# Performance work log

Measured on AMD Instinct MI355X. Metric: run time of the kernel, lower is better.

The kernel has to match this reference:

```python
import jax, jax.numpy as jnp
import numpy as np

HIDDEN = 1024
TILE = 128


def setup_inputs() -> dict:
    key = jax.random.key(0)
    ks = jax.random.split(key, 9)
    B, S, D = 2, 4096, HIDDEN
    s = 1.0 / np.sqrt(D)
    return {
        "batch": jax.random.normal(ks[0], (B, S, D), jnp.float32),
        "Wq": jax.random.normal(ks[1], (D, D), jnp.float32) * s,
        "bq": jax.random.normal(ks[2], (D,), jnp.float32) * 0.01,
        "Wk": jax.random.normal(ks[3], (D, D), jnp.float32) * s,
        "bk": jax.random.normal(ks[4], (D,), jnp.float32) * 0.01,
        "Wv": jax.random.normal(ks[5], (D, D), jnp.float32) * s,
        "bv": jax.random.normal(ks[6], (D,), jnp.float32) * 0.01,
        "Wo": jax.random.normal(ks[7], (D, D), jnp.float32) * s,
        "bo": jax.random.normal(ks[8], (D,), jnp.float32) * 0.01,
    }


def reference(batch, Wq, bq, Wk, bk, Wv, bv, Wo, bo):
    B, S, D = batch.shape
    scale = 1.0 / np.sqrt(D)
    T = S // TILE  # seq_len chosen divisible by tile size

    # Projections (nn.Linear: x @ W.T + b)
    q = batch @ Wq.T + bq
    k = batch @ Wk.T + bk
    v = batch @ Wv.T + bv

    # Tile K/V along the sequence axis: [B, T, TILE, D]
    k_t = k.reshape(B, T, TILE, D)
    v_t = v.reshape(B, T, TILE, D)

    # Per-tile scores and per-tile softmax (NOT a global softmax —
    # faithful to the module, which normalizes within each kv tile).
    scores = jnp.einsum("bqd,btkd->btqk", q, k_t) * scale  # [B, T, S, TILE]
    w = jax.nn.softmax(scores, axis=-1)

    # Sum of per-tile attention outputs over kv tiles
    out = jnp.einsum("btqk,btkd->bqd", w, v_t)  # [B, S, D]

    # Normalizing factor: sum of per-tile softmax weights (== T analytically,
    # computed explicitly to match the original math bit-for-bit in spirit)
    norm = w.sum(axis=-1).sum(axis=1)[..., None]  # [B, S, 1]
    out = out / (norm + 1e-6)

    return out @ Wo.T + bo
```

## Files before the change

### kernel.cpp

```cpp
#include <hip/hip_runtime.h>


#define D_ 1024
#define S_ 4096
#define B_ 2

typedef unsigned short u16;
typedef float f32x4 __attribute__((ext_vector_type(4)));
typedef float float4v __attribute__((ext_vector_type(4)));
typedef __bf16 bf16x8 __attribute__((ext_vector_type(8)));
typedef unsigned short us8 __attribute__((ext_vector_type(8)));

static __device__ __forceinline__ u16 f2bf(float f) {
    unsigned int u = __builtin_bit_cast(unsigned int, f);
    u += 0x7FFFu + ((u >> 16) & 1u);
    return (u16)(u >> 16);
}

static __device__ __forceinline__ void gld16(const u16* g, u16* l) {
    __builtin_amdgcn_global_load_lds(
        (const __attribute__((address_space(1))) void*)g,
        (__attribute__((address_space(3))) void*)l, 16, 0, 0);
}

template <int N>
static __device__ __forceinline__ void waitv() {
    if constexpr (N == 0)      asm volatile("s_waitcnt vmcnt(0)" ::: "memory");
    else if constexpr (N == 2) asm volatile("s_waitcnt vmcnt(2)" ::: "memory");
    else if constexpr (N == 6) asm volatile("s_waitcnt vmcnt(6)" ::: "memory");
}

static __device__ __forceinline__ void lgkm0sb() {
    asm volatile("s_waitcnt lgkmcnt(0)" ::: "memory");
    __builtin_amdgcn_sched_barrier(0);
}

static __device__ __forceinline__ void xcd_map(int& bx, int& by) {
    const int gx = gridDim.x, gy = gridDim.y;
    int lin = blockIdx.x + blockIdx.y * gx;
    int ry = gy >> 3;
    int idx = lin >> 3;
    int q = idx / ry;
    bx = q;
    by = (lin & 7) * ry + (idx - q * ry);
}

__global__ void cast_kernel(const float* __restrict__ in, u16* __restrict__ out, int n8) {
    int i = blockIdx.x * blockDim.x + threadIdx.x;
    int stride = gridDim.x * blockDim.x;
    for (; i < n8; i += stride) {
        const float4v* p = (const float4v*)in + 2 * (size_t)i;
        float4v a = p[0], b = p[1];
        us8 o;
        o[0] = f2bf(a[0]); o[1] = f2bf(a[1]); o[2] = f2bf(a[2]); o[3] = f2bf(a[3]);
        o[4] = f2bf(b[0]); o[5] = f2bf(b[1]); o[6] = f2bf(b[2]); o[7] = f2bf(b[3]);
        *((us8*)out + i) = o;
    }
}

__global__ void cast4_kernel(const float* __restrict__ w0, const float* __restrict__ w1,
                             const float* __restrict__ w2, const float* __restrict__ w3,
                             u16* __restrict__ out, int n8per) {
    const float* srcs[4] = {w0, w1, w2, w3};
    const float* in = srcs[blockIdx.y];
    u16* o = out + (size_t)blockIdx.y * (size_t)n8per * 8;
    int i = blockIdx.x * blockDim.x + threadIdx.x;
    int stride = gridDim.x * blockDim.x;
    for (; i < n8per; i += stride) {
        const float4v* p = (const float4v*)in + 2 * (size_t)i;
        float4v a = p[0], b = p[1];
        us8 v;
        v[0] = f2bf(a[0]); v[1] = f2bf(a[1]); v[2] = f2bf(a[2]); v[3] = f2bf(a[3]);
        v[4] = f2bf(b[0]); v[5] = f2bf(b[1]); v[6] = f2bf(b[2]); v[7] = f2bf(b[3]);
        *((us8*)o + i) = v;
    }
}

__global__ void concat_bias(const float* __restrict__ b0, const float* __restrict__ b1,
                            const float* __restrict__ b2, float* __restrict__ out) {
    int i = blockIdx.x * 256 + threadIdx.x;
    const float* s = (i < 1024) ? b0 : ((i < 2048) ? b1 : b2);
    out[i] = s[i & 1023];
}

__global__ void transpose_v(const u16* __restrict__ V, u16* __restrict__ Vt, int ldv) {
    __shared__ u16 t[64][72];
    const int tid = threadIdx.x;
    const int d0 = blockIdx.x * 64;
    const int s0 = blockIdx.y * 64;
    const u16* Vb = V + (size_t)blockIdx.z * ((size_t)S_ * ldv);
    u16* Vtb = Vt + (size_t)blockIdx.z * ((size_t)D_ * S_);
#pragma unroll
    for (int it = 0; it < 2; it++) {
        int idx = it * 256 + tid;
        int row = idx >> 3;
        int ch = idx & 7;
        us8 v = *(const us8*)&Vb[(size_t)(s0 + row) * ldv + d0 + ch * 8];
        *(us8*)&t[row][ch * 8] = v;
    }
    __syncthreads();
#pragma unroll
    for (int it = 0; it < 2; it++) {
        int idx = it * 256 + tid;
        int jj = idx >> 3;
        int ch = idx & 7;
        us8 v;
#pragma unroll
        for (int e = 0; e < 8; e++) v[e] = t[ch * 8 + e][jj];
        *(us8*)&Vtb[(size_t)(d0 + jj) * S_ + s0 + ch * 8] = v;
    }
}

#define MMQ(ACC, MB, NB)                                                      \
    {                                                                         \
        _Pragma("unroll") for (int mi_ = 0; mi_ < 4; ++mi_) {                 \
            _Pragma("unroll") for (int ni_ = 0; ni_ < 2; ++ni_) {             \
                _Pragma("unroll") for (int kh_ = 0; kh_ < 2; ++kh_) {         \
                    ACC[(MB) + mi_][(NB) + ni_] =                             \
                        __builtin_amdgcn_mfma_f32_16x16x32_bf16(              \
                            af[mi_][kh_], bf[ni_][kh_],                       \
                            ACC[(MB) + mi_][(NB) + ni_], 0, 0, 0);            \
                }                                                             \
            }                                                                 \
        }                                                                     \
    }

__global__ __launch_bounds__(512, 1) void gemm_sm256(
    const u16* __restrict__ A, const u16* __restrict__ B, u16* __restrict__ C,
    int K, int lda, int ldb, int ldc, long sA, long sB, long sC)
{
    __shared__ u16 lA[2][256 * 64];
    __shared__ u16 lB[2][256 * 64];
    __shared__ float sred[2][8][128];
    const int tid = threadIdx.x, lane = tid & 63, wid = tid >> 6;
    const int wr = wid >> 2, wc = wid & 3;
    const int ar = lane & 15, sl = lane >> 4;
    const int z = blockIdx.z;
    A += (size_t)z * sA;
    B += (size_t)z * sB;
    int bx, by;
    xcd_map(bx, by);
    const int m0 = by * 256, n0 = bx * 256;
    const int NT = K >> 6, NI = NT >> 1;

    f32x4 acc[8][4];
#pragma unroll
    for (int i = 0; i < 8; i++)
#pragma unroll
        for (int j = 0; j < 4; j++)
#pragma unroll
            for (int r = 0; r < 4; r++) acc[i][j][r] = 0.0f;

    auto stg = [&](const u16* __restrict__ M, int ld, int mb, u16* ld0, int t, int h) {
#pragma unroll
        for (int j = 0; j < 2; ++j) {
            const int u = j * 512 + wid * 64 + lane;
            const int row = h * 128 + (u >> 3);
            const int ls = (u & 7) ^ (row & 7);
            gld16(M + (size_t)(mb + row) * ld + (t << 6) + ls * 8, ld0 + h * 8192 + u * 8);
        }
    };
    auto rd = [&](const u16* l, int R, int kh) -> bf16x8 {
        const int ps = ((kh << 2) | sl) ^ (R & 7);
        return *(const bf16x8*)&l[R * 64 + ps * 8];
    };

    stg(A, lda, m0, lA[0], 0, 0); stg(A, lda, m0, lA[0], 0, 1);
    stg(B, ldb, n0, lB[0], 0, 0); stg(B, ldb, n0, lB[0], 0, 1);
    stg(A, lda, m0, lA[1], 1, 0);
    waitv<2>();
    __builtin_amdgcn_s_barrier();

    bf16x8 af[4][2], bf[2][2];
    for (int j = 0; j < NI; ++j) {
        const int a = 2 * j, b = a + 1;
        const bool s2 = (j + 1 < NI);
#pragma unroll
        for (int mi = 0; mi < 4; ++mi)
#pragma unroll
            for (int kh = 0; kh < 2; ++kh)
                af[mi][kh] = rd(lA[0], wr * 128 + mi * 16 + ar, kh);
#pragma unroll
        for (int ni = 0; ni < 2; ++ni)
#pragma unroll
            for (int kh = 0; kh < 2; ++kh)
                bf[ni][kh] = rd(lB[0], wc * 64 + ni * 16 + ar, kh);
        stg(A, lda, m0, lA[1], b, 1);
        lgkm0sb();
        __builtin_amdgcn_s_setprio(1);
        MMQ(acc, 0, 0);
        __builtin_amdgcn_s_setprio(0);
        __builtin_amdgcn_s_barrier();
#pragma unroll
        for (int ni = 0; ni < 2; ++ni)
#pragma unroll
            for (int kh = 0; kh < 2; ++kh)
                bf[ni][kh] = rd(lB[0], wc * 64 + (2 + ni) * 16 + ar, kh);
        stg(B, ldb, n0, lB[1], b, 0);
        lgkm0sb();
        __builtin_amdgcn_s_setprio(1);
        MMQ(acc, 0, 2);
        __builtin_amdgcn_s_setprio(0);
        __builtin_amdgcn_s_barrier();
#pragma unroll
        for (int mi = 0; mi < 4; ++mi)
#pragma unroll
            for (int kh = 0; kh < 2; ++kh)
                af[mi][kh] = rd(lA[0], wr * 128 + (4 + mi) * 16 + ar, kh);
        stg(B, ldb, n0, lB[1], b, 1);
        lgkm0sb();
        __builtin_amdgcn_s_setprio(1);
        MMQ(acc, 4, 2);
        __builtin_amdgcn_s_setprio(0);
        __builtin_amdgcn_s_barrier();
#pragma unroll
        for (int ni = 0; ni < 2; ++ni)
#pragma unroll
            for (int kh = 0; kh < 2; ++kh)
                bf[ni][kh] = rd(lB[0], wc * 64 + ni * 16 + ar, kh);
        if (s2) stg(A, lda, m0, lA[0], a + 2, 0);
        lgkm0sb();
        __builtin_amdgcn_s_setprio(1);
        MMQ(acc, 4, 0);
        __builtin_amdgcn_s_setprio(0);
        if (s2) waitv<2>(); else waitv<0>();
        __builtin_amdgcn_s_barrier();
#pragma unroll
        for (int mi = 0; mi < 4; ++mi)
#pragma unroll
            for (int kh = 0; kh < 2; ++kh)
                af[mi][kh] = rd(lA[1], wr * 128 + mi * 16 + ar, kh);
#pragma unroll
        for (int ni = 0; ni < 2; ++ni)
#pragma unroll
            for (int kh = 0; kh < 2; ++kh)
                bf[ni][kh] = rd(lB[1], wc * 64 + ni * 16 + ar, kh);
        if (s2) stg(B, ldb, n0, lB[0], a + 2, 0);
        lgkm0sb();
        __builtin_amdgcn_s_setprio(1);
        MMQ(acc, 0, 0);
        __builtin_amdgcn_s_setprio(0);
        __builtin_amdgcn_s_barrier();
#pragma unroll
        for (int ni = 0; ni < 2; ++ni)
#pragma unroll
            for (int kh = 0; kh < 2; ++kh)
                bf[ni][kh] = rd(lB[1], wc * 64 + (2 + ni) * 16 + ar, kh);
        if (s2) stg(B, ldb, n0, lB[0], a + 2, 1);
        lgkm0sb();
        __builtin_amdgcn_s_setprio(1);
        MMQ(acc, 0, 2);
        __builtin_amdgcn_s_setprio(0);
        __builtin_amdgcn_s_barrier();
#pragma unroll
        for (int mi = 0; mi < 4; ++mi)
#pragma unroll
            for (int kh = 0; kh < 2; ++kh)
                af[mi][kh] = rd(lA[1], wr * 128 + (4 + mi) * 16 + ar, kh);
        if (s2) stg(A, lda, m0, lA[0], a + 2, 1);
        lgkm0sb();
        __builtin_amdgcn_s_setprio(1);
        MMQ(acc, 4, 2);
        __builtin_amdgcn_s_setprio(0);
        __builtin_amdgcn_s_barrier();
#pragma unroll
        for (int ni = 0; ni < 2; ++ni)
#pragma unroll
            for (int kh = 0; kh < 2; ++kh)
                bf[ni][kh] = rd(lB[1], wc * 64 + ni * 16 + ar, kh);
        if (s2) stg(A, lda, m0, lA[1], b + 2, 0);
        lgkm0sb();
        __builtin_amdgcn_s_setprio(1);
        MMQ(acc, 4, 0);
        __builtin_amdgcn_s_setprio(0);
        if (s2) waitv<2>(); else waitv<0>();
        __builtin_amdgcn_s_barrier();
    }

    const float SL = 0.03125f * 1.44269504088896341f;
#pragma unroll
    for (int mi = 0; mi < 8; mi++) {
#pragma unroll
        for (int r = 0; r < 4; r++) {
            float m = acc[mi][0][r];
#pragma unroll
            for (int ni = 1; ni < 4; ni++) m = fmaxf(m, acc[mi][ni][r]);
            m = fmaxf(m, __shfl_xor(m, 1));
            m = fmaxf(m, __shfl_xor(m, 2));
            m = fmaxf(m, __shfl_xor(m, 4));
            m = fmaxf(m, __shfl_xor(m, 8));
            if (ar == 0) sred[0][wid][mi * 16 + sl * 4 + r] = m;
        }
    }
    __syncthreads();
#pragma unroll
    for (int mi = 0; mi < 8; mi++) {
#pragma unroll
        for (int r = 0; r < 4; r++) {
            const int rl = mi * 16 + sl * 4 + r;
            const float mc = fmaxf(sred[0][wid][rl], sred[0][wid ^ 1][rl]);
            float s = 0.0f;
#pragma unroll
            for (int ni = 0; ni < 4; ni++) {
                float e = exp2f((acc[mi][ni][r] - mc) * SL);
                acc[mi][ni][r] = e;
                s += e;
            }
            s += __shfl_xor(s, 1);
            s += __shfl_xor(s, 2);
            s += __shfl_xor(s, 4);
            s += __shfl_xor(s, 8);
            if (ar == 0) sred[1][wid][rl] = s;
        }
    }
    __syncthreads();
    u16* Cp = C + (size_t)z * sC;
#pragma unroll
    for (int mi = 0; mi < 8; mi++) {
#pragma unroll
        for (int r = 0; r < 4; r++) {
            const int rl = mi * 16 + sl * 4 + r;
            const float inv = 1.0f / (sred[1][wid][rl] + sred[1][wid ^ 1][rl]);
            const int row = m0 + wr * 128 + rl;
#pragma unroll
            for (int ni = 0; ni < 4; ni++)
                Cp[(size_t)row * ldc + n0 + wc * 64 + ni * 16 + ar] =
                    f2bf(acc[mi][ni][r] * inv);
        }
    }
}

template <int EPI>
__global__ __launch_bounds__(512, 1) void gemm128(
    const u16* __restrict__ A, const u16* __restrict__ B, void* __restrict__ Cv,
    const float* __restrict__ bias, int K, int lda, int ldb, int ldc,
    long sA, long sB, long sC, float scale)
{
    __shared__ u16 lA[3][128 * 64];
    __shared__ u16 lB[3][256 * 64];
    const int tid = threadIdx.x, lane = tid & 63, wid = tid >> 6;
    const int wr = wid >> 2, wc = wid & 3;
    const int ar = lane & 15, sl = lane >> 4;
    const int z = blockIdx.z;
    A += (size_t)z * sA;
    B += (size_t)z * sB;
    int bx, by;
    xcd_map(bx, by);
    const int m0 = by * 128, n0 = bx * 256;
    const int NT = K >> 6;

    f32x4 acc[4][4];
#pragma unroll
    for (int i = 0; i < 4; i++)
#pragma unroll
        for (int j = 0; j < 4; j++)
#pragma unroll
            for (int r = 0; r < 4; r++) acc[i][j][r] = 0.0f;

    auto stgA = [&](int t) {
        u16* dst = &lA[t % 3][0];
#pragma unroll
        for (int j = 0; j < 2; ++j) {
            const int u = j * 512 + wid * 64 + lane;
            const int row = u >> 3;
            const int ls = (u & 7) ^ (row & 7);
            gld16(A + (size_t)(m0 + row) * lda + (t << 6) + ls * 8, dst + u * 8);
        }
    };
    auto stgB = [&](int t, int h) {
        u16* dst = &lB[t % 3][0];
#pragma unroll
        for (int j = 0; j < 2; ++j) {
            const int u = j * 512 + wid * 64 + lane;
            const int row = h * 128 + (u >> 3);
            const int ls = (u & 7) ^ (row & 7);
            gld16(B + (size_t)(n0 + row) * ldb + (t << 6) + ls * 8, dst + h * 8192 + u * 8);
        }
    };
    auto rd = [&](const u16* l, int R, int kh) -> bf16x8 {
        const int ps = ((kh << 2) | sl) ^ (R & 7);
        return *(const bf16x8*)&l[R * 64 + ps * 8];
    };

    stgA(0); stgB(0, 0); stgB(0, 1);
    stgA(1); stgB(1, 0); stgB(1, 1);
    waitv<6>();
    __builtin_amdgcn_s_barrier();

    bf16x8 af[4][2], bf[2][2];
    for (int t = 0; t < NT; ++t) {
        const u16* bufA = &lA[t % 3][0];
        const u16* bufB = &lB[t % 3][0];
        const bool s2 = (t + 2 < NT);
#pragma unroll
        for (int mi = 0; mi < 4; ++mi)
#pragma unroll
            for (int kh = 0; kh < 2; ++kh)
                af[mi][kh] = rd(bufA, wr * 64 + mi * 16 + ar, kh);
#pragma unroll
        for (int ni = 0; ni < 2; ++ni)
#pragma unroll
            for (int kh = 0; kh < 2; ++kh)
                bf[ni][kh] = rd(bufB, wc * 64 + ni * 16 + ar, kh);
        if (s2) { stgA(t + 2); stgB(t + 2, 0); }
        lgkm0sb();
        __builtin_amdgcn_s_setprio(1);
        MMQ(acc, 0, 0);
        __builtin_amdgcn_s_setprio(0);
        __builtin_amdgcn_s_barrier();
#pragma unroll
        for (int ni = 0; ni < 2; ++ni)
#pragma unroll
            for (int kh = 0; kh < 2; ++kh)
                bf[ni][kh] = rd(bufB, wc * 64 + (2 + ni) * 16 + ar, kh);
        if (s2) stgB(t + 2, 1);
        lgkm0sb();
        __builtin_amdgcn_s_setprio(1);
        MMQ(acc, 0, 2);
        __builtin_amdgcn_s_setprio(0);
        if (s2) waitv<6>(); else waitv<0>();
        __builtin_amdgcn_s_barrier();
    }

#pragma unroll
    for (int mi = 0; mi < 4; mi++) {
#pragma unroll
        for (int ni = 0; ni < 4; ni++) {
            const int col = n0 + wc * 64 + ni * 16 + ar;
            const int rowb = m0 + wr * 64 + mi * 16 + sl * 4;
            if constexpr (EPI == 0) {
                u16* C = (u16*)Cv + (size_t)z * sC;
                const float bv = bias[col];
#pragma unroll
                for (int r = 0; r < 4; r++)
                    C[(size_t)(rowb + r) * ldc + col] = f2bf(acc[mi][ni][r] + bv);
            } else if constexpr (EPI == 1) {
                u16* C = (u16*)Cv + (size_t)z * sC;
#pragma unroll
                for (int r = 0; r < 4; r++)
                    C[(size_t)(rowb + r) * ldc + col] = f2bf(acc[mi][ni][r] * scale);
            } else {
                float* C = (float*)Cv + (size_t)z * sC;
                const float bv = bias[col];
#pragma unroll
                for (int r = 0; r < 4; r++)
                    C[(size_t)(rowb + r) * ldc + col] = acc[mi][ni][r] + bv;
            }
        }
    }
}

extern "C" void kernel_launch(void* const* d_in, const int* in_sizes, int n_in,
                              void* d_out, int out_size, void* d_ws, size_t ws_size,
                              hipStream_t stream)
{
    const float* X  = (const float*)d_in[0];
    const float* Wq = (const float*)d_in[1];
    const float* bq = (const float*)d_in[2];
    const float* Wk = (const float*)d_in[3];
    const float* bk = (const float*)d_in[4];
    const float* Wv = (const float*)d_in[5];
    const float* bv = (const float*)d_in[6];
    const float* Wo = (const float*)d_in[7];
    const float* bo = (const float*)d_in[8];
    float* OUT = (float*)d_out;

    u16* ws = (u16*)d_ws;
    const size_t NTOK = (size_t)B_ * S_;
    const size_t XSZ = NTOK * D_;
    u16* Xb   = ws;
    u16* QKVb = Xb + XSZ;
    u16* Vt   = QKVb + NTOK * (size_t)(3 * D_);
    u16* Wqb  = Vt + XSZ;
    u16* Wsm  = Wqb + (size_t)4 * D_ * D_;
    float* bqkv = (float*)(Wsm + (size_t)B_ * S_ * S_);
    u16* Ob   = Xb;

    u16* Qp = QKVb;
    u16* Kp = QKVb + D_;
    u16* Vp = QKVb + 2 * D_;
    const int ldqkv = 3 * D_;

    cast_kernel<<<dim3(2048), dim3(256), 0, stream>>>(X, Xb, (int)(XSZ / 8));
    cast4_kernel<<<dim3(512, 4), dim3(256), 0, stream>>>(Wq, Wk, Wv, Wo, Wqb,
                                                         (int)((size_t)D_ * D_ / 8));
    concat_bias<<<dim3(12), dim3(256), 0, stream>>>(bq, bk, bv, bqkv);

    gemm128<0><<<dim3(3 * D_ / 256, NTOK / 128, 1), 512, 0, stream>>>(
        Xb, Wqb, QKVb, bqkv, D_, D_, D_, ldqkv, 0, 0, 0, 1.0f);

    transpose_v<<<dim3(D_ / 64, S_ / 64, B_), 256, 0, stream>>>(Vp, Vt, ldqkv);

    gemm_sm256<<<dim3(S_ / 256, S_ / 256, B_), 512, 0, stream>>>(
        Qp, Kp, Wsm, D_, ldqkv, ldqkv, S_,
        (long)S_ * ldqkv, (long)S_ * ldqkv, (long)S_ * S_);

    gemm128<1><<<dim3(D_ / 256, S_ / 128, B_), 512, 0, stream>>>(
        Wsm, Vt, Ob, nullptr, S_, S_, S_, D_,
        (long)S_ * S_, (long)D_ * S_, (long)S_ * D_, 1.0f / (32.0f + 1e-6f));

    gemm128<2><<<dim3(D_ / 256, NTOK / 128, 1), 512, 0, stream>>>(
        Ob, Wqb + (size_t)3 * D_ * D_, OUT, bo, D_, D_, D_, D_, 0, 0, 0, 1.0f);
}
```

Before: 372.7 us.

## Generalize 256x256 GEMM with full B-fragment reuse and use it for QKV projection

The 256x256 softmax GEMM becomes a templated gemm256 with an epilogue switch. Its inner loop now loads all four B fragments once per K-step and reuses them across both A halves instead of reloading B, with precomputed staging and read addresses and a reordered prefetch schedule. The QKV projection moves from the 128-row GEMM to this 256x256 tile kernel, halving its grid. This cuts LDS traffic and raises per-block reuse, at the cost of more registers held for fragments and fewer blocks for the projection.

```diff
diff --git a/kernel.cpp b/kernel.cpp
--- a/kernel.cpp
+++ b/kernel.cpp
@@ -26,7 +26,6 @@
 template <int N>
 static __device__ __forceinline__ void waitv() {
     if constexpr (N == 0)      asm volatile("s_waitcnt vmcnt(0)" ::: "memory");
-    else if constexpr (N == 2) asm volatile("s_waitcnt vmcnt(2)" ::: "memory");
     else if constexpr (N == 6) asm volatile("s_waitcnt vmcnt(6)" ::: "memory");
 }
 
@@ -111,23 +110,25 @@
     }
 }
 
-#define MMQ(ACC, MB, NB)                                                      \
+#define MM8(MI0, NI0)                                                         \
     {                                                                         \
         _Pragma("unroll") for (int mi_ = 0; mi_ < 4; ++mi_) {                 \
             _Pragma("unroll") for (int ni_ = 0; ni_ < 2; ++ni_) {             \
                 _Pragma("unroll") for (int kh_ = 0; kh_ < 2; ++kh_) {         \
-                    ACC[(MB) + mi_][(NB) + ni_] =                             \
+                    acc[(MI0) + mi_][(NI0) + ni_] =                           \
                         __builtin_amdgcn_mfma_f32_16x16x32_bf16(              \
-                            af[mi_][kh_], bf[ni_][kh_],                       \
-                            ACC[(MB) + mi_][(NB) + ni_], 0, 0, 0);            \
+                            af[(MI0) + mi_][kh_], bf[(NI0) + ni_][kh_],       \
+                            acc[(MI0) + mi_][(NI0) + ni_], 0, 0, 0);          \
                 }                                                             \
             }                                                                 \
         }                                                                     \
     }
 
-__global__ __launch_bounds__(512, 1) void gemm_sm256(
-    const u16* __restrict__ A, const u16* __restrict__ B, u16* __restrict__ C,
-    int K, int lda, int ldb, int ldc, long sA, long sB, long sC)
+template <int EPI>
+__global__ __launch_bounds__(512, 1) void gemm256(
+    const u16* __restrict__ A, const u16* __restrict__ B, void* __restrict__ Cv,
+    const float* __restrict__ bias, int K, int lda, int ldb, int ldc,
+    long sA, long sB, long sC)
 {
     __shared__ u16 lA[2][256 * 64];
     __shared__ u16 lB[2][256 * 64];
@@ -151,181 +152,180 @@
 #pragma unroll
             for (int r = 0; r < 4; r++) acc[i][j][r] = 0.0f;
 
-    auto stg = [&](const u16* __restrict__ M, int ld, int mb, u16* ld0, int t, int h) {
-#pragma unroll
-        for (int j = 0; j < 2; ++j) {
-            const int u = j * 512 + wid * 64 + lane;
-            const int row = h * 128 + (u >> 3);
-            const int ls = (u & 7) ^ (row & 7);
-            gld16(M + (size_t)(mb + row) * ld + (t << 6) + ls * 8, ld0 + h * 8192 + u * 8);
-        }
-    };
-    auto rd = [&](const u16* l, int R, int kh) -> bf16x8 {
-        const int ps = ((kh << 2) | sl) ^ (R & 7);
-        return *(const bf16x8*)&l[R * 64 + ps * 8];
-    };
-
-    stg(A, lda, m0, lA[0], 0, 0); stg(A, lda, m0, lA[0], 0, 1);
-    stg(B, ldb, n0, lB[0], 0, 0); stg(B, ldb, n0, lB[0], 0, 1);
-    stg(A, lda, m0, lA[1], 1, 0);
-    waitv<2>();
+    const int uS = wid * 64 + lane;
+    const int rS = uS >> 3;
+    const int lsS = (lane & 7) ^ (rS & 7);
+    const u16* pA = A + (size_t)(m0 + rS) * lda + lsS * 8;
+    const u16* pB = B + (size_t)(n0 + rS) * ldb + lsS * 8;
+    auto stgA = [&](int t, int h) {
+        u16* dst = &lA[t & 1][h * 8192 + uS * 8];
+        const u16* src = pA + (size_t)h * 128 * lda + (t << 6);
+        gld16(src, dst);
+        gld16(src + (size_t)64 * lda, dst + 4096);
+    };
+    auto stgB = [&](int t, int h) {
+        u16* dst = &lB[t & 1][h * 8192 + uS * 8];
+        const u16* src = pB + (size_t)h * 128 * ldb + (t << 6);
+        gld16(src, dst);
+        gld16(src + (size_t)64 * ldb, dst + 4096);
+    };
+    const int psk0 = (sl ^ (ar & 7)) * 8;
+    const int psk1 = ((4 | sl) ^ (ar & 7)) * 8;
+    const int aoff = wr * 8192 + ar * 64;
+    const int boff = (wc >> 1) * 8192 + (wc & 1) * 4096 + ar * 64;
+    auto rdA = [&](int buf, int mi, int kh) -> bf16x8 {
+        return *(const bf16x8*)&lA[buf][aoff + mi * 1024 + (kh ? psk1 : psk0)];
+    };
+    auto rdB = [&](int buf, int ni, int kh) -> bf16x8 {
+        return *(const bf16x8*)&lB[buf][boff + ni * 1024 + (kh ? psk1 : psk0)];
+    };
+
+    stgA(0, 0); stgA(0, 1); stgB(0, 0); stgB(0, 1);
+    stgB(1, 0); stgB(1, 1); stgA(1, 0);
+    waitv<6>();
     __builtin_amdgcn_s_barrier();
 
-    bf16x8 af[4][2], bf[2][2];
+    bf16x8 af[8][2], bf[4][2];
     for (int j = 0; j < NI; ++j) {
         const int a = 2 * j, b = a + 1;
-        const bool s2 = (j + 1 < NI);
+        const bool more = (j + 1 < NI);
 #pragma unroll
         for (int mi = 0; mi < 4; ++mi)
 #pragma unroll
-            for (int kh = 0; kh < 2; ++kh)
-                af[mi][kh] = rd(lA[0], wr * 128 + mi * 16 + ar, kh);
-#pragma unroll
-        for (int ni = 0; ni < 2; ++ni)
-#pragma unroll
-            for (int kh = 0; kh < 2; ++kh)
-                bf[ni][kh] = rd(lB[0], wc * 64 + ni * 16 + ar, kh);
-        stg(A, lda, m0, lA[1], b, 1);
+            for (int kh = 0; kh < 2; ++kh) af[mi][kh] = rdA(0, mi, kh);
+#pragma unroll
+        for (int ni = 0; ni < 4; ++ni)
+#pragma unroll
+            for (int kh = 0; kh < 2; ++kh) bf[ni][kh] = rdB(0, ni, kh);
+        stgA(b, 1);
         lgkm0sb();
         __builtin_amdgcn_s_setprio(1);
-        MMQ(acc, 0, 0);
-        __builtin_amdgcn_s_setprio(0);
-        __builtin_amdgcn_s_barrier();
-#pragma unroll
-        for (int ni = 0; ni < 2; ++ni)
-#pragma unroll
-            for (int kh = 0; kh < 2; ++kh)
-                bf[ni][kh] = rd(lB[0], wc * 64 + (2 + ni) * 16 + ar, kh);
-        stg(B, ldb, n0, lB[1], b, 0);
+        MM8(0, 0);
+        __builtin_amdgcn_s_setprio(0);
+        __builtin_amdgcn_s_barrier();
+#pragma unroll
+        for (int mi = 4; mi < 8; ++mi)
+#pragma unroll
+            for (int kh = 0; kh < 2; ++kh) af[mi][kh] = rdA(0, mi, kh);
+        if (more) stgB(a + 2, 0);
         lgkm0sb();
         __builtin_amdgcn_s_setprio(1);
-        MMQ(acc, 0, 2);
-        __builtin_amdgcn_s_setprio(0);
+        MM8(4, 0);
+        __builtin_amdgcn_s_setprio(0);
+        __builtin_amdgcn_s_barrier();
+        if (more) stgB(a + 2, 1);
+        __builtin_amdgcn_s_setprio(1);
+        MM8(0, 2);
+        __builtin_amdgcn_s_setprio(0);
+        __builtin_amdgcn_s_barrier();
+        if (more) stgA(a + 2, 0);
+        __builtin_amdgcn_s_setprio(1);
+        MM8(4, 2);
+        __builtin_amdgcn_s_setprio(0);
+        if (more) waitv<6>(); else waitv<0>();
         __builtin_amdgcn_s_barrier();
 #pragma unroll
         for (int mi = 0; mi < 4; ++mi)
 #pragma unroll
-            for (int kh = 0; kh < 2; ++kh)
-                af[mi][kh] = rd(lA[0], wr * 128 + (4 + mi) * 16 + ar, kh);
-        stg(B, ldb, n0, lB[1], b, 1);
+            for (int kh = 0; kh < 2; ++kh) af[mi][kh] = rdA(1, mi, kh);
+#pragma unroll
+        for (int ni = 0; ni < 4; ++ni)
+#pragma unroll
+            for (int kh = 0; kh < 2; ++kh) bf[ni][kh] = rdB(1, ni, kh);
+        if (more) stgA(a + 2, 1);
         lgkm0sb();
         __builtin_amdgcn_s_setprio(1);
-        MMQ(acc, 4, 2);
-        __builtin_amdgcn_s_setprio(0);
-        __builtin_amdgcn_s_barrier();
-#pragma unroll
-        for (int ni = 0; ni < 2; ++ni)
-#pragma unroll
-            for (int kh = 0; kh < 2; ++kh)
-                bf[ni][kh] = rd(lB[0], wc * 64 + ni * 16 + ar, kh);
-        if (s2) stg(A, lda, m0, lA[0], a + 2, 0);
+        MM8(0, 0);
+        __builtin_amdgcn_s_setprio(0);
+        __builtin_amdgcn_s_barrier();
+#pragma unroll
+        for (int mi = 4; mi < 8; ++mi)
+#pragma unroll
+            for (int kh = 0; kh < 2; ++kh) af[mi][kh] = rdA(1, mi, kh);
+        if (more) stgB(b + 2, 0);
         lgkm0sb();
         __builtin_amdgcn_s_setprio(1);
-        MMQ(acc, 4, 0);
-        __builtin_amdgcn_s_setprio(0);
-        if (s2) waitv<2>(); else waitv<0>();
-        __builtin_amdgcn_s_barrier();
-#pragma unroll
-        for (int mi = 0; mi < 4; ++mi)
-#pragma unroll
-            for (int kh = 0; kh < 2; ++kh)
-                af[mi][kh] = rd(lA[1], wr * 128 + mi * 16 + ar, kh);
-#pragma unroll
-        for (int ni = 0; ni < 2; ++ni)
-#pragma unroll
-            for (int kh = 0; kh < 2; ++kh)
-                bf[ni][kh] = rd(lB[1], wc * 64 + ni * 16 + ar, kh);
-        if (s2) stg(B, ldb, n0, lB[0], a + 2, 0);
-        lgkm0sb();
-        __builtin_amdgcn_s_setprio(1);
-        MMQ(acc, 0, 0);
-        __builtin_amdgcn_s_setprio(0);
-        __builtin_amdgcn_s_barrier();
-#pragma unroll
-        for (int ni = 0; ni < 2; ++ni)
-#pragma unroll
-            for (int kh = 0; kh < 2; ++kh)
-                bf[ni][kh] = rd(lB[1], wc * 64 + (2 + ni) * 16 + ar, kh);
-        if (s2) stg(B, ldb, n0, lB[0], a + 2, 1);
-        lgkm0sb();
-        __builtin_amdgcn_s_setprio(1);
-        MMQ(acc, 0, 2);
-        __builtin_amdgcn_s_setprio(0);
-        __builtin_amdgcn_s_barrier();
-#pragma unroll
-        for (int mi = 0; mi < 4; ++mi)
-#pragma unroll
-            for (int kh = 0; kh < 2; ++kh)
-                af[mi][kh] = rd(lA[1], wr * 128 + (4 + mi) * 16 + ar, kh);
-        if (s2) stg(A, lda, m0, lA[0], a + 2, 1);
-        lgkm0sb();
-        __builtin_amdgcn_s_setprio(1);
-        MMQ(acc, 4, 2);
-        __builtin_amdgcn_s_setprio(0);
-        __builtin_amdgcn_s_barrier();
-#pragma unroll
-        for (int ni = 0; ni < 2; ++ni)
-#pragma unroll
-            for (int kh = 0; kh < 2; ++kh)
-                bf[ni][kh] = rd(lB[1], wc * 64 + ni * 16 + ar, kh);
-        if (s2) stg(A, lda, m0, lA[1], b + 2, 0);
-        lgkm0sb();
-        __builtin_amdgcn_s_setprio(1);
-        MMQ(acc, 4, 0);
-        __builtin_amdgcn_s_setprio(0);
-        if (s2) waitv<2>(); else waitv<0>();
-        __builtin_amdgcn_s_barrier();
-    }
-
-    const float SL = 0.03125f * 1.44269504088896341f;
-#pragma unroll
-    for (int mi = 0; mi < 8; mi++) {
-#pragma unroll
-        for (int r = 0; r < 4; r++) {
-            float m = acc[mi][0][r];
-#pragma unroll
-            for (int ni = 1; ni < 4; ni++) m = fmaxf(m, acc[mi][ni][r]);
-            m = fmaxf(m, __shfl_xor(m, 1));
-            m = fmaxf(m, __shfl_xor(m, 2));
-            m = fmaxf(m, __shfl_xor(m, 4));
-            m = fmaxf(m, __shfl_xor(m, 8));
-            if (ar == 0) sred[0][wid][mi * 16 + sl * 4 + r] = m;
-        }
-    }
-    __syncthreads();
-#pragma unroll
-    for (int mi = 0; mi < 8; mi++) {
-#pragma unroll
-        for (int r = 0; r < 4; r++) {
-            const int rl = mi * 16 + sl * 4 + r;
-            const float mc = fmaxf(sred[0][wid][rl], sred[0][wid ^ 1][rl]);
-            float s = 0.0f;
+        MM8(4, 0);
+        __builtin_amdgcn_s_setprio(0);
+        __builtin_amdgcn_s_barrier();
+        if (more) stgB(b + 2, 1);
+        __builtin_amdgcn_s_setprio(1);
+        MM8(0, 2);
+        __builtin_amdgcn_s_setprio(0);
+        __builtin_amdgcn_s_barrier();
+        if (more) stgA(b + 2, 0);
+        __builtin_amdgcn_s_setprio(1);
+        MM8(4, 2);
+        __builtin_amdgcn_s_setprio(0);
+        if (more) waitv<6>(); else waitv<0>();
+        __builtin_amdgcn_s_barrier();
+    }
+
+    if constexpr (EPI == 3) {
+        const float SL = 0.03125f * 1.44269504088896341f;
+#pragma unroll
+        for (int mi = 0; mi < 8; mi++) {
+#pragma unroll
+            for (int r = 0; r < 4; r++) {
+                float m = acc[mi][0][r];
+#pragma unroll
+                for (int ni = 1; ni < 4; ni++) m = fmaxf(m, acc[mi][ni][r]);
+                m = fmaxf(m, __shfl_xor(m, 1));
+                m = fmaxf(m, __shfl_xor(m, 2));
+                m = fmaxf(m, __shfl_xor(m, 4));
+                m = fmaxf(m, __shfl_xor(m, 8));
+                if (ar == 0) sred[0][wid][mi * 16 + sl * 4 + r] = m;
+            }
+        }
+        __syncthreads();
+#pragma unroll
+        for (int mi = 0; mi < 8; mi++) {
+#pragma unroll
+            for (int r = 0; r < 4; r++) {
+                const int rl = mi * 16 + sl * 4 + r;
+                const float mc = fmaxf(sred[0][wid][rl], sred[0][wid ^ 1][rl]);
+                float s = 0.0f;
+#pragma unroll
+                for (int ni = 0; ni < 4; ni++) {
+                    float e = exp2f((acc[mi][ni][r] - mc) * SL);
+                    acc[mi][ni][r] = e;
+                    s += e;
+                }
+                s += __shfl_xor(s, 1);
+                s += __shfl_xor(s, 2);
+                s += __shfl_xor(s, 4);
+                s += __shfl_xor(s, 8);
+                if (ar == 0) sred[1][wid][rl] = s;
+            }
+        }
+        __syncthreads();
+        u16* C = (u16*)Cv + (size_t)z * sC;
+#pragma unroll
+        for (int mi = 0; mi < 8; mi++) {
+#pragma unroll
+            for (int r = 0; r < 4; r++) {
+                const int rl = mi * 16 + sl * 4 + r;
+                const float inv = 1.0f / (sred[1][wid][rl] + sred[1][wid ^ 1][rl]);
+                const int row = m0 + wr * 128 + rl;
+#pragma unroll
+                for (int ni = 0; ni < 4; ni++)
+                    C[(size_t)row * ldc + n0 + wc * 64 + ni * 16 + ar] =
+                        f2bf(acc[mi][ni][r] * inv);
+            }
+        }
+    } else {
+        u16* C = (u16*)Cv + (size_t)z * sC;
+#pragma unroll
+        for (int mi = 0; mi < 8; mi++) {
 #pragma unroll
             for (int ni = 0; ni < 4; ni++) {
-                float e = exp2f((acc[mi][ni][r] - mc) * SL);
-                acc[mi][ni][r] = e;
-                s += e;
+                const int col = n0 + wc * 64 + ni * 16 + ar;
+                const int rowb = m0 + wr * 128 + mi * 16 + sl * 4;
+                const float bv = bias[col];
+#pragma unroll
+                for (int r = 0; r < 4; r++)
+                    C[(size_t)(rowb + r) * ldc + col] = f2bf(acc[mi][ni][r] + bv);
             }
-            s += __shfl_xor(s, 1);
-            s += __shfl_xor(s, 2);
-            s += __shfl_xor(s, 4);
-            s += __shfl_xor(s, 8);
-            if (ar == 0) sred[1][wid][rl] = s;
-        }
-    }
-    __syncthreads();
-    u16* Cp = C + (size_t)z * sC;
-#pragma unroll
-    for (int mi = 0; mi < 8; mi++) {
-#pragma unroll
-        for (int r = 0; r < 4; r++) {
-            const int rl = mi * 16 + sl * 4 + r;
-            const float inv = 1.0f / (sred[1][wid][rl] + sred[1][wid ^ 1][rl]);
-            const int row = m0 + wr * 128 + rl;
-#pragma unroll
-            for (int ni = 0; ni < 4; ni++)
-                Cp[(size_t)row * ldc + n0 + wc * 64 + ni * 16 + ar] =
-                    f2bf(acc[mi][ni][r] * inv);
         }
     }
 }
@@ -405,7 +405,14 @@
         if (s2) { stgA(t + 2); stgB(t + 2, 0); }
         lgkm0sb();
         __builtin_amdgcn_s_setprio(1);
-        MMQ(acc, 0, 0);
+#pragma unroll
+        for (int mi = 0; mi < 4; ++mi)
+#pragma unroll
+            for (int ni = 0; ni < 2; ++ni)
+#pragma unroll
+                for (int kh = 0; kh < 2; ++kh)
+                    acc[mi][ni] = __builtin_amdgcn_mfma_f32_16x16x32_bf16(
+                        af[mi][kh], bf[ni][kh], acc[mi][ni], 0, 0, 0);
         __builtin_amdgcn_s_setprio(0);
         __builtin_amdgcn_s_barrier();
 #pragma unroll
@@ -416,7 +423,14 @@
         if (s2) stgB(t + 2, 1);
         lgkm0sb();
         __builtin_amdgcn_s_setprio(1);
-        MMQ(acc, 0, 2);
+#pragma unroll
+        for (int mi = 0; mi < 4; ++mi)
+#pragma unroll
+            for (int ni = 0; ni < 2; ++ni)
+#pragma unroll
+                for (int kh = 0; kh < 2; ++kh)
+                    acc[mi][2 + ni] = __builtin_amdgcn_mfma_f32_16x16x32_bf16(
+                        af[mi][kh], bf[ni][kh], acc[mi][2 + ni], 0, 0, 0);
         __builtin_amdgcn_s_setprio(0);
         if (s2) waitv<6>(); else waitv<0>();
         __builtin_amdgcn_s_barrier();
@@ -428,13 +442,7 @@
         for (int ni = 0; ni < 4; ni++) {
             const int col = n0 + wc * 64 + ni * 16 + ar;
             const int rowb = m0 + wr * 64 + mi * 16 + sl * 4;
-            if constexpr (EPI == 0) {
-                u16* C = (u16*)Cv + (size_t)z * sC;
-                const float bv = bias[col];
-#pragma unroll
-                for (int r = 0; r < 4; r++)
-                    C[(size_t)(rowb + r) * ldc + col] = f2bf(acc[mi][ni][r] + bv);
-            } else if constexpr (EPI == 1) {
+            if constexpr (EPI == 1) {
                 u16* C = (u16*)Cv + (size_t)z * sC;
 #pragma unroll
                 for (int r = 0; r < 4; r++)
@@ -486,13 +494,13 @@
                                                          (int)((size_t)D_ * D_ / 8));
     concat_bias<<<dim3(12), dim3(256), 0, stream>>>(bq, bk, bv, bqkv);
 
-    gemm128<0><<<dim3(3 * D_ / 256, NTOK / 128, 1), 512, 0, stream>>>(
-        Xb, Wqb, QKVb, bqkv, D_, D_, D_, ldqkv, 0, 0, 0, 1.0f);
+    gemm256<0><<<dim3(3 * D_ / 256, NTOK / 256, 1), 512, 0, stream>>>(
+        Xb, Wqb, QKVb, bqkv, D_, D_, D_, ldqkv, 0, 0, 0);
 
     transpose_v<<<dim3(D_ / 64, S_ / 64, B_), 256, 0, stream>>>(Vp, Vt, ldqkv);
 
-    gemm_sm256<<<dim3(S_ / 256, S_ / 256, B_), 512, 0, stream>>>(
-        Qp, Kp, Wsm, D_, ldqkv, ldqkv, S_,
+    gemm256<3><<<dim3(S_ / 256, S_ / 256, B_), 512, 0, stream>>>(
+        Qp, Kp, Wsm, nullptr, D_, ldqkv, ldqkv, S_,
         (long)S_ * ldqkv, (long)S_ * ldqkv, (long)S_ * S_);
 
     gemm128<1><<<dim3(D_ / 256, S_ / 128, B_), 512, 0, stream>>>(
```

Result: no change. 370.7 us (-0.5%).
